# Kernel optimization log

Hardware: AMD Instinct MI355X
Metric: run time of the kernel (lower is better)

Reference implementation:

```python
import jax, jax.numpy as jnp
import numpy as np

D_MODEL = 2048
NUM_HEADS = 32
NUM_KV_HEADS = 8
D_K = D_MODEL // NUM_HEADS  # 64
GROUPS = NUM_HEADS // NUM_KV_HEADS  # 4
KV_DIM = NUM_KV_HEADS * D_K  # 512


def setup_inputs() -> dict:
    key = jax.random.key(0)
    ks = jax.random.split(key, 9)
    s = 0.02
    return {
        "x": jax.random.normal(ks[0], (2, 2048, D_MODEL), dtype=jnp.float32),
        "Wq": jax.random.normal(ks[1], (D_MODEL, D_MODEL), dtype=jnp.float32) * s,
        "bq": jnp.zeros((D_MODEL,), dtype=jnp.float32),
        "Wk": jax.random.normal(ks[2], (D_MODEL, KV_DIM), dtype=jnp.float32) * s,
        "bk": jnp.zeros((KV_DIM,), dtype=jnp.float32),
        "Wv": jax.random.normal(ks[3], (D_MODEL, KV_DIM), dtype=jnp.float32) * s,
        "bv": jnp.zeros((KV_DIM,), dtype=jnp.float32),
        "Wo": jax.random.normal(ks[4], (D_MODEL, D_MODEL), dtype=jnp.float32) * s,
        "bo": jnp.zeros((D_MODEL,), dtype=jnp.float32),
    }


def reference(x, Wq, bq, Wk, bk, Wv, bv, Wo, bo):
    B, S, _ = x.shape
    # projections
    Q = (x @ Wq + bq).reshape(B, S, NUM_HEADS, D_K).transpose(0, 2, 1, 3)      # [B,H,S,dk]
    K = (x @ Wk + bk).reshape(B, S, NUM_KV_HEADS, D_K).transpose(0, 2, 1, 3)   # [B,Hkv,S,dk]
    V = (x @ Wv + bv).reshape(B, S, NUM_KV_HEADS, D_K).transpose(0, 2, 1, 3)
    # repeat_interleave KV heads to match query heads
    K = jnp.repeat(K, GROUPS, axis=1)  # [B,H,S,dk]
    V = jnp.repeat(V, GROUPS, axis=1)
    scale = 1.0 / jnp.sqrt(jnp.asarray(D_K, dtype=x.dtype))
    scores = jnp.einsum("bhqd,bhkd->bhqk", Q, K) * scale  # [B,H,S,S]
    attn = jax.nn.softmax(scores, axis=-1)
    out = jnp.einsum("bhqk,bhkd->bhqd", attn, V)           # [B,H,S,dk]
    out = out.transpose(0, 2, 1, 3).reshape(B, S, D_MODEL)
    return out @ Wo + bo
```

## Files before the change

kernel.cpp:

```cpp
#include <hip/hip_runtime.h>
#include <hip/hip_bf16.h>
#include <stdint.h>

typedef __bf16 bf16;
typedef __bf16 bf16x8 __attribute__((ext_vector_type(8)));
typedef float  f32x2  __attribute__((ext_vector_type(2)));
typedef float  f32x4  __attribute__((ext_vector_type(4)));
typedef float  f32x16 __attribute__((ext_vector_type(16)));

#define D_MODEL 2048
#define KV_DIM  512
#define SEQ     2048
#define BATCH   2
#define MTOT    (BATCH*SEQ)
#define QKV_N   3072
#define QSCALE  (0.125f*1.44269504088896f)

#if __has_builtin(__builtin_amdgcn_exp2f)
#define EXP2(x) __builtin_amdgcn_exp2f(x)
#else
#define EXP2(x) exp2f(x)
#endif

__global__ __launch_bounds__(256) void cvt_f32_bf16(const float* __restrict__ in,
                                                    bf16* __restrict__ out, int n) {
  int i = (blockIdx.x * 256 + threadIdx.x) * 4;
  if (i < n) {
    float4 v = *reinterpret_cast<const float4*>(in + i);
    bf16 o[4] = {(bf16)v.x, (bf16)v.y, (bf16)v.z, (bf16)v.w};
    *reinterpret_cast<uint64_t*>(out + i) = *reinterpret_cast<const uint64_t*>(o);
  }
}

__global__ __launch_bounds__(256) void transpose_all(
    const float* __restrict__ Wq, const float* __restrict__ Wk,
    const float* __restrict__ Wv, const float* __restrict__ Wo,
    bf16* __restrict__ Wall, bf16* __restrict__ Wot) {
  const int z = blockIdx.z;
  const float* W; bf16* dst; int N;
  if (z == 0)      { W = Wq; dst = Wall;                          N = 2048; }
  else if (z == 1) { W = Wk; dst = Wall + (size_t)2048 * 2048;    N = 512;  }
  else if (z == 2) { W = Wv; dst = Wall + (size_t)2560 * 2048;    N = 512;  }
  else             { W = Wo; dst = Wot;                           N = 2048; }
  const int n0 = blockIdx.x * 64, k0 = blockIdx.y * 64;
  if (n0 >= N) return;
  __shared__ float tile[64][65];
  const int tx = threadIdx.x & 63;
  const int ty = threadIdx.x >> 6;
  #pragma unroll
  for (int i = ty; i < 64; i += 4)
    tile[i][tx] = W[(size_t)(k0 + i) * N + n0 + tx];
  __syncthreads();
  #pragma unroll
  for (int i = ty; i < 64; i += 4)
    dst[(size_t)(n0 + i) * 2048 + k0 + tx] = (bf16)tile[tx][i];
}

__global__ __launch_bounds__(256) void transpose_v(const bf16* __restrict__ QKV,
                                                   bf16* __restrict__ Vtg) {
  __shared__ bf16 t[64][72];
  const int st = blockIdx.x;
  const int bk = blockIdx.y;
  const int b = bk >> 3, kvh = bk & 7;
  const int tid = threadIdx.x;
  const int r = tid >> 2, c = (tid & 3) * 16;
  const bf16* src = QKV + (size_t)(b * SEQ + st * 64 + r) * QKV_N + 2560 + kvh * 64 + c;
  *(bf16x8*)&t[r][c]     = *(const bf16x8*)src;
  *(bf16x8*)&t[r][c + 8] = *(const bf16x8*)(src + 8);
  __syncthreads();
  bf16 tmp[16];
  #pragma unroll
  for (int j = 0; j < 16; ++j) tmp[j] = t[c + j][r];
  bf16* dst = Vtg + (size_t)(bk * 64 + r) * SEQ + st * 64 + c;
  *(bf16x8*)dst       = *(const bf16x8*)tmp;
  *(bf16x8*)(dst + 8) = *(const bf16x8*)(tmp + 8);
}

__device__ __forceinline__ void gload_lds16(const bf16* g, bf16* l) {
  __builtin_amdgcn_global_load_lds(
      (const __attribute__((address_space(1))) uint32_t*)g,
      (__attribute__((address_space(3))) uint32_t*)l, 16, 0, 0);
}

__device__ __forceinline__ uint32_t pk2(float a, float b) {
  union { bf16 h[2]; uint32_t u; } v;
  v.h[0] = (bf16)a; v.h[1] = (bf16)b;
  return v.u;
}

template<int NF, int OUT_BF16>
__global__ __launch_bounds__(512, 2) void gemm256(
    const bf16* __restrict__ A, const bf16* __restrict__ Bt,
    const float* __restrict__ b0, const float* __restrict__ b1,
    const float* __restrict__ b2, int sp1, int sp2, int nscale, float scale,
    void* __restrict__ Cout, int N, int K)
{
  __shared__ bf16 As[2][256 * 64];
  __shared__ bf16 Bs[2][NF * 64 * 64];

  const int tid = threadIdx.x, lane = tid & 63;
  const int wid = tid >> 6;
  const int wr = wid >> 2, wc = wid & 3;
  const int l15 = lane & 15, hi = lane >> 4;
  const int rx = l15 & 7;

  const int bid = blockIdx.y * 16 + blockIdx.x;
  const int swz = (bid & 7) * 32 + (bid >> 3);
  const int m0 = (swz >> 4) * 256, n0 = (swz & 15) * (NF * 16 * 4);

  const int srow = tid >> 3;
  const int schk = (tid & 7) ^ (srow & 7);
  const bf16* aSrc = A  + (size_t)(m0 + srow) * K + schk * 8;
  const bf16* bSrc = Bt + (size_t)(n0 + srow) * K + schk * 8;
  const size_t rstep = (size_t)64 * K;

  f32x4 acc[8][NF] = {};

  const int NT = K / 64;

#define G256_STAGE(T, BUF)                                            \
  {                                                                   \
    const bf16* a_ = aSrc + (T) * 64;                                 \
    _Pragma("unroll")                                                 \
    for (int j = 0; j < 4; ++j)                                       \
      gload_lds16(a_ + j * rstep, &As[BUF][j * 4096 + tid * 8]);      \
    const bf16* b_ = bSrc + (T) * 64;                                 \
    _Pragma("unroll")                                                 \
    for (int j = 0; j < NF; ++j)                                      \
      gload_lds16(b_ + j * rstep, &Bs[BUF][j * 4096 + tid * 8]);      \
  }

#define G256_WAITL()                                                  \
  if constexpr (NF == 3) asm volatile("s_waitcnt vmcnt(7)" ::: "memory"); \
  else                   asm volatile("s_waitcnt vmcnt(6)" ::: "memory");

#define G256_BODY(BUF)                                                \
  {                                                                   \
    _Pragma("unroll")                                                 \
    for (int kk = 0; kk < 2; ++kk) {                                  \
      bf16x8 af[8], bfv[NF];                                          \
      _Pragma("unroll")                                               \
      for (int m = 0; m < 8; ++m)                                     \
        af[m] = *(const bf16x8*)&As[BUF][(wr * 128 + m * 16 + l15) * 64 \
                                         + ((kk * 4 + hi) ^ rx) * 8];  \
      _Pragma("unroll")                                               \
      for (int n = 0; n < NF; ++n)                                    \
        bfv[n] = *(const bf16x8*)&Bs[BUF][(wc * (NF * 16) + n * 16 + l15) * 64 \
                                          + ((kk * 4 + hi) ^ rx) * 8]; \
      __builtin_amdgcn_s_setprio(1);                                  \
      _Pragma("unroll")                                               \
      for (int m = 0; m < 8; ++m)                                     \
        _Pragma("unroll")                                             \
        for (int n = 0; n < NF; ++n)                                  \
          acc[m][n] = __builtin_amdgcn_mfma_f32_16x16x32_bf16(        \
              af[m], bfv[n], acc[m][n], 0, 0, 0);                     \
      __builtin_amdgcn_s_setprio(0);                                  \
    }                                                                 \
  }

  G256_STAGE(0, 0)
  G256_STAGE(1, 1)
  G256_WAITL()
  __builtin_amdgcn_sched_barrier(0);
  __builtin_amdgcn_s_barrier();
  __builtin_amdgcn_sched_barrier(0);

  for (int t = 0; t < NT; t += 2) {
    #pragma unroll
    for (int u = 0; u < 2; ++u) {
      G256_BODY(u)
      __builtin_amdgcn_sched_barrier(0);
      __builtin_amdgcn_s_barrier();
      __builtin_amdgcn_sched_barrier(0);
      const int tt = t + u;
      if (tt < NT - 2) {
        G256_STAGE(tt + 2, u)
        G256_WAITL()
      } else {
        asm volatile("s_waitcnt vmcnt(0)" ::: "memory");
      }
      __builtin_amdgcn_sched_barrier(0);
      __builtin_amdgcn_s_barrier();
      __builtin_amdgcn_sched_barrier(0);
    }
  }

#undef G256_STAGE
#undef G256_WAITL
#undef G256_BODY

  const int rbase = m0 + wr * 128 + hi * 4;
  const int cb = n0 + wc * (NF * 16) + l15;
  #pragma unroll
  for (int n = 0; n < NF; ++n) {
    const int col = cb + n * 16;
    float bv;
    if (col < sp1)      bv = b0[col];
    else if (col < sp2) bv = b1[col - sp1];
    else                bv = b2[col - sp2];
    const float scl = (col < nscale) ? scale : 1.0f;
    #pragma unroll
    for (int m = 0; m < 8; ++m) {
      const int rb = rbase + m * 16;
      #pragma unroll
      for (int r = 0; r < 4; ++r) {
        const float v = (acc[m][n][r] + bv) * scl;
        if (OUT_BF16) ((bf16*)Cout)[(size_t)(rb + r) * N + col] = (bf16)v;
        else          ((float*)Cout)[(size_t)(rb + r) * N + col] = v;
      }
    }
  }
}

__global__ __launch_bounds__(256) void attn_kernel(
    const bf16* __restrict__ QKV, const bf16* __restrict__ Vtg, bf16* __restrict__ ctx)
{
  __shared__ bf16 smem[4][64 * 64];

  const int tid = threadIdx.x, lane = tid & 63, wid = tid >> 6;
  const int l31 = lane & 31, hi = lane >> 5;
  const int qt = blockIdx.x & 15;
  const int bh = blockIdx.x >> 4;
  const int h = bh & 31, b = bh >> 5, kvh = h >> 2;

  const bf16* gK = QKV + (size_t)b * SEQ * QKV_N + 2048 + kvh * 64;
  const bf16* gV = Vtg + (size_t)(b * 8 + kvh) * 64 * SEQ;

  const int sr  = lane >> 3;
  const int scn = (lane & 7) ^ sr;

  bf16x8 qf[4];
  {
    const bf16* qp = QKV + (size_t)(b * SEQ + qt * 128 + wid * 32 + l31) * QKV_N + h * 64 + hi * 8;
    #pragma unroll
    for (int kt = 0; kt < 4; ++kt) qf[kt] = *(const bf16x8*)(qp + kt * 16);
  }

  bf16x8 onesv;
  #pragma unroll
  for (int j = 0; j < 8; ++j) onesv[j] = (bf16)1.0f;

  f32x16 o0 = {}, o1 = {};
  f32x16 lacc = {};

  const int row0 = (wid * 2 + 0) * 8 + sr;
  const int row1 = (wid * 2 + 1) * 8 + sr;
  const bf16* pK0 = gK + (size_t)row0 * QKV_N + scn * 8;
  const bf16* pK1 = gK + (size_t)row1 * QKV_N + scn * 8;
  const bf16* pV0 = gV + (size_t)row0 * SEQ + scn * 8;
  const bf16* pV1 = gV + (size_t)row1 * SEQ + scn * 8;

  gload_lds16(pK0, &smem[0][(wid * 2 + 0) * 512]);
  gload_lds16(pK1, &smem[0][(wid * 2 + 1) * 512]);
  gload_lds16(pV0, &smem[2][(wid * 2 + 0) * 512]);
  gload_lds16(pV1, &smem[2][(wid * 2 + 1) * 512]);
  pK0 += (size_t)64 * QKV_N; pK1 += (size_t)64 * QKV_N; pV0 += 64; pV1 += 64;
  __syncthreads();

  const int rx = l31 & 7;

  for (int it = 0; it < 32; ++it) {
    const int cur = it & 1;
    if (it < 31) {
      gload_lds16(pK0, &smem[cur ^ 1][(wid * 2 + 0) * 512]);
      gload_lds16(pK1, &smem[cur ^ 1][(wid * 2 + 1) * 512]);
      gload_lds16(pV0, &smem[2 + (cur ^ 1)][(wid * 2 + 0) * 512]);
      gload_lds16(pV1, &smem[2 + (cur ^ 1)][(wid * 2 + 1) * 512]);
      pK0 += (size_t)64 * QKV_N; pK1 += (size_t)64 * QKV_N; pV0 += 64; pV1 += 64;
    }
    const bf16* Kb = smem[cur];
    const bf16* Vb = smem[2 + cur];

    bf16x8 kf[8];
    #pragma unroll
    for (int kt = 0; kt < 4; ++kt) {
      const int ck = hi + 2 * kt;
      kf[kt]     = *(const bf16x8*)(Kb + (size_t)l31 * 64        + ((ck ^ rx) * 8));
      kf[kt + 4] = *(const bf16x8*)(Kb + (size_t)(32 + l31) * 64 + ((ck ^ rx) * 8));
    }
    f32x16 s0v = {}, s1v = {};
    __builtin_amdgcn_s_setprio(1);
    #pragma unroll
    for (int kt = 0; kt < 4; ++kt) {
      s0v = __builtin_amdgcn_mfma_f32_32x32x16_bf16(kf[kt],     qf[kt], s0v, 0, 0, 0);
      s1v = __builtin_amdgcn_mfma_f32_32x32x16_bf16(kf[kt + 4], qf[kt], s1v, 0, 0, 0);
    }
    __builtin_amdgcn_s_setprio(0);

    bf16x8 vf[8];
    #pragma unroll
    for (int s = 0; s < 4; ++s) {
      const int ck = hi + 2 * s;
      vf[s]     = *(const bf16x8*)(Vb + (size_t)l31 * 64        + ((ck ^ rx) * 8));
      vf[s + 4] = *(const bf16x8*)(Vb + (size_t)(32 + l31) * 64 + ((ck ^ rx) * 8));
    }

    #pragma unroll
    for (int r = 0; r < 16; ++r) { s0v[r] = EXP2(s0v[r]); s1v[r] = EXP2(s1v[r]); }

    #pragma unroll
    for (int s = 0; s < 4; ++s) {
      const f32x16& sv = (s < 2) ? s0v : s1v;
      const int rb = (s & 1) * 8;
      uint32_t Aw = pk2(sv[rb + 0], sv[rb + 1]);
      uint32_t Bw = pk2(sv[rb + 2], sv[rb + 3]);
      uint32_t Cw = pk2(sv[rb + 4], sv[rb + 5]);
      uint32_t Dw = pk2(sv[rb + 6], sv[rb + 7]);
      union { uint32_t w[4]; bf16x8 v; } pf;
#if __has_builtin(__builtin_amdgcn_permlane32_swap)
      auto rA = __builtin_amdgcn_permlane32_swap(Aw, Cw, false, false);
      auto rB = __builtin_amdgcn_permlane32_swap(Bw, Dw, false, false);
      pf.w[0] = rA[0]; pf.w[1] = rB[0]; pf.w[2] = rA[1]; pf.w[3] = rB[1];
#else
      uint32_t U = hi ? Aw : Cw;
      uint32_t W = hi ? Bw : Dw;
      uint32_t pU = (uint32_t)__shfl_xor((int)U, 32);
      uint32_t pW = (uint32_t)__shfl_xor((int)W, 32);
      pf.w[0] = hi ? pU : Aw;
      pf.w[1] = hi ? pW : Bw;
      pf.w[2] = hi ? Cw : pU;
      pf.w[3] = hi ? Dw : pW;
#endif
      __builtin_amdgcn_s_setprio(1);
      o0 = __builtin_amdgcn_mfma_f32_32x32x16_bf16(vf[s],     pf.v, o0, 0, 0, 0);
      o1 = __builtin_amdgcn_mfma_f32_32x32x16_bf16(vf[s + 4], pf.v, o1, 0, 0, 0);
      lacc = __builtin_amdgcn_mfma_f32_32x32x16_bf16(onesv,   pf.v, lacc, 0, 0, 0);
      __builtin_amdgcn_s_setprio(0);
    }
    __syncthreads();
  }

  const float inv = 1.0f / lacc[0];
  o0 *= inv; o1 *= inv;

  uint32_t* ot = (uint32_t*)((bf16*)smem + wid * 2304);
  #pragma unroll
  for (int r = 0; r < 16; r += 2) {
    const int d = (r & 3) + 8 * (r >> 2) + 4 * hi;
    ot[l31 * 36 + (d >> 1)]        = pk2(o0[r], o0[r + 1]);
    ot[l31 * 36 + ((32 + d) >> 1)] = pk2(o1[r], o1[r + 1]);
  }
  __syncthreads();
  {
    const int q2 = lane >> 1, hf = lane & 1;
    const bf16* src = (const bf16*)smem + wid * 2304 + q2 * 72 + hf * 32;
    bf16* dst = ctx + (size_t)(b * SEQ + qt * 128 + wid * 32 + q2) * D_MODEL + h * 64 + hf * 32;
    #pragma unroll
    for (int k = 0; k < 4; ++k)
      *(bf16x8*)(dst + k * 8) = *(const bf16x8*)(src + k * 8);
  }
}

extern "C" void kernel_launch(void* const* d_in, const int* in_sizes, int n_in,
                              void* d_out, int out_size, void* d_ws, size_t ws_size,
                              hipStream_t stream) {
  const float* x  = (const float*)d_in[0];
  const float* Wq = (const float*)d_in[1];
  const float* bq = (const float*)d_in[2];
  const float* Wk = (const float*)d_in[3];
  const float* bk = (const float*)d_in[4];
  const float* Wv = (const float*)d_in[5];
  const float* bv = (const float*)d_in[6];
  const float* Wo = (const float*)d_in[7];
  const float* bo = (const float*)d_in[8];
  float* out = (float*)d_out;

  char* ws = (char*)d_ws;
  size_t off = 0;
  bf16* xb   = (bf16*)(ws + off); off += (size_t)MTOT * D_MODEL * 2;
  bf16* Wall = (bf16*)(ws + off); off += (size_t)QKV_N * D_MODEL * 2;
  bf16* Wot  = (bf16*)(ws + off); off += (size_t)D_MODEL * D_MODEL * 2;
  bf16* QKV  = (bf16*)(ws + off); off += (size_t)MTOT * QKV_N * 2;
  bf16* ctx  = (bf16*)(ws + off); off += (size_t)MTOT * D_MODEL * 2;
  bf16* Vtg  = (bf16*)(ws + off); off += (size_t)16 * 64 * SEQ * 2;

  {
    int n = MTOT * D_MODEL;
    cvt_f32_bf16<<<n / 4 / 256, 256, 0, stream>>>(x, xb, n);
  }
  transpose_all<<<dim3(32, 32, 4), 256, 0, stream>>>(Wq, Wk, Wv, Wo, Wall, Wot);

  gemm256<3, 1><<<dim3(16, 16), 512, 0, stream>>>(
      xb, Wall, bq, bk, bv, 2048, 2560, 2048, QSCALE, QKV, QKV_N, D_MODEL);

  transpose_v<<<dim3(SEQ / 64, 16), 256, 0, stream>>>(QKV, Vtg);

  attn_kernel<<<dim3((SEQ / 128) * BATCH * 32), 256, 0, stream>>>(QKV, Vtg, ctx);

  gemm256<2, 0><<<dim3(16, 16), 512, 0, stream>>>(
      ctx, Wot, bo, bo, bo, 2048, 2048, 0, 1.0f, out, D_MODEL, D_MODEL);
}
```

Baseline: 239.2 us.

## Switch GEMM to 32x32x16 MFMA with 4x2 wave tiling

Reorganizes the 256-wide GEMM so each of the 8 waves covers a 64-row by NF*32-column subtile using 32x32x16 bf16 MFMAs instead of 16x16x32. This changes the wave grid from 2x4 to 4x2, the LDS fragment read pattern and the epilogue row mapping. The larger MFMA shape needs fewer LDS fragment loads per MFMA and fewer instructions per tile. In exchange the swizzle and XOR pattern for LDS reads changes, which may alter bank conflicts.

```diff
diff --git a/kernel.cpp b/kernel.cpp
--- a/kernel.cpp
+++ b/kernel.cpp
@@ -100,13 +100,13 @@
 
   const int tid = threadIdx.x, lane = tid & 63;
   const int wid = tid >> 6;
-  const int wr = wid >> 2, wc = wid & 3;
-  const int l15 = lane & 15, hi = lane >> 4;
-  const int rx = l15 & 7;
+  const int wr = wid >> 1, wc = wid & 1;
+  const int l31 = lane & 31, hi2 = lane >> 5;
+  const int rx = l31 & 7;
 
   const int bid = blockIdx.y * 16 + blockIdx.x;
   const int swz = (bid & 7) * 32 + (bid >> 3);
-  const int m0 = (swz >> 4) * 256, n0 = (swz & 15) * (NF * 16 * 4);
+  const int m0 = (swz >> 4) * 256, n0 = (swz & 15) * (NF * 64);
 
   const int srow = tid >> 3;
   const int schk = (tid & 7) ^ (srow & 7);
@@ -114,7 +114,7 @@
   const bf16* bSrc = Bt + (size_t)(n0 + srow) * K + schk * 8;
   const size_t rstep = (size_t)64 * K;
 
-  f32x4 acc[8][NF] = {};
+  f32x16 acc[2][NF] = {};
 
   const int NT = K / 64;
 
@@ -137,22 +137,22 @@
 #define G256_BODY(BUF)                                                \
   {                                                                   \
     _Pragma("unroll")                                                 \
-    for (int kk = 0; kk < 2; ++kk) {                                  \
-      bf16x8 af[8], bfv[NF];                                          \
+    for (int ks = 0; ks < 4; ++ks) {                                  \
+      bf16x8 af[2], bfv[NF];                                          \
       _Pragma("unroll")                                               \
-      for (int m = 0; m < 8; ++m)                                     \
-        af[m] = *(const bf16x8*)&As[BUF][(wr * 128 + m * 16 + l15) * 64 \
-                                         + ((kk * 4 + hi) ^ rx) * 8];  \
+      for (int m = 0; m < 2; ++m)                                     \
+        af[m] = *(const bf16x8*)&As[BUF][(wr * 64 + m * 32 + l31) * 64 \
+                                         + (((ks * 2 + hi2) ^ rx) * 8)]; \
       _Pragma("unroll")                                               \
       for (int n = 0; n < NF; ++n)                                    \
-        bfv[n] = *(const bf16x8*)&Bs[BUF][(wc * (NF * 16) + n * 16 + l15) * 64 \
-                                          + ((kk * 4 + hi) ^ rx) * 8]; \
+        bfv[n] = *(const bf16x8*)&Bs[BUF][(wc * (NF * 32) + n * 32 + l31) * 64 \
+                                          + (((ks * 2 + hi2) ^ rx) * 8)]; \
       __builtin_amdgcn_s_setprio(1);                                  \
       _Pragma("unroll")                                               \
-      for (int m = 0; m < 8; ++m)                                     \
+      for (int m = 0; m < 2; ++m)                                     \
         _Pragma("unroll")                                             \
         for (int n = 0; n < NF; ++n)                                  \
-          acc[m][n] = __builtin_amdgcn_mfma_f32_16x16x32_bf16(        \
+          acc[m][n] = __builtin_amdgcn_mfma_f32_32x32x16_bf16(        \
               af[m], bfv[n], acc[m][n], 0, 0, 0);                     \
       __builtin_amdgcn_s_setprio(0);                                  \
     }                                                                 \
@@ -189,24 +189,24 @@
 #undef G256_WAITL
 #undef G256_BODY
 
-  const int rbase = m0 + wr * 128 + hi * 4;
-  const int cb = n0 + wc * (NF * 16) + l15;
+  const int cb = n0 + wc * (NF * 32) + l31;
   #pragma unroll
   for (int n = 0; n < NF; ++n) {
-    const int col = cb + n * 16;
+    const int col = cb + n * 32;
     float bv;
     if (col < sp1)      bv = b0[col];
     else if (col < sp2) bv = b1[col - sp1];
     else                bv = b2[col - sp2];
     const float scl = (col < nscale) ? scale : 1.0f;
     #pragma unroll
-    for (int m = 0; m < 8; ++m) {
-      const int rb = rbase + m * 16;
+    for (int m = 0; m < 2; ++m) {
+      const int rb = m0 + wr * 64 + m * 32 + 4 * hi2;
       #pragma unroll
-      for (int r = 0; r < 4; ++r) {
+      for (int r = 0; r < 16; ++r) {
+        const int row = rb + (r & 3) + 8 * (r >> 2);
         const float v = (acc[m][n][r] + bv) * scl;
-        if (OUT_BF16) ((bf16*)Cout)[(size_t)(rb + r) * N + col] = (bf16)v;
-        else          ((float*)Cout)[(size_t)(rb + r) * N + col] = v;
+        if (OUT_BF16) ((bf16*)Cout)[(size_t)row * N + col] = (bf16)v;
+        else          ((float*)Cout)[(size_t)row * N + col] = v;
       }
     }
   }
```

Result: no change. 235.0 us (median of 2 runs) (-1.8%).
